# Optimization experiments

Measured on AMD Instinct MI355X. Metric: run time of the kernel, lower is better.

## Reference

```python
import jax, jax.numpy as jnp
import numpy as np

B, C, N, K, R, PART = 2, 64, 16384, 16, 16, 6
_reps = [C // PART] * (PART - 1) + [C - (C // PART) * (PART - 1)]
_RIDX = np.repeat(np.arange(PART), _reps)  # torch.repeat_interleave index map (6 -> C)


def setup_inputs() -> dict:
    key = jax.random.key(0)
    ks = jax.random.split(key, 26)
    f = lambda i, sh: jax.random.normal(ks[i], sh, jnp.float32)
    u = lambda i, sh: jax.random.uniform(ks[i], sh, jnp.float32, 0.5, 1.5)
    return {
        'x': f(0, (B, C, N)),
        'xyz': f(1, (B, 3, N)) * 0.5,
        'idx': jax.random.randint(ks[2], (B, N, K), 0, N),
        'w3a': f(3, (C, 1, 3, 3, 3)) * 0.1, 'b3a': f(4, (C,)) * 0.1,
        'g3a': u(5, (C,)), 'be3a': f(6, (C,)) * 0.1, 'm3a': f(7, (C,)) * 0.1, 'v3a': u(8, (C,)),
        'w3b': f(9, (C, 1, 3, 3, 3)) * 0.1, 'b3b': f(10, (C,)) * 0.1,
        'g3b': u(11, (C,)), 'be3b': f(12, (C,)) * 0.1, 'm3b': f(13, (C,)) * 0.1, 'v3b': u(14, (C,)),
        'wp1': f(15, (3, C)) * 0.1, 'gp': u(16, (3,)), 'bp': f(17, (3,)) * 0.1,
        'mp': f(18, (3,)) * 0.1, 'vp': u(19, (3,)),
        'wp2': f(20, (3, 3)) * 0.3,
        'gt': u(21, (C,)), 'bt': f(22, (C,)) * 0.1, 'mt': f(23, (C,)) * 0.1, 'vt': u(24, (C,)),
    }


def _bn(x, g, b, m, v, eps):
    sh = (1, -1) + (1,) * (x.ndim - 2)
    return (x - m.reshape(sh)) * (g.reshape(sh) * jax.lax.rsqrt(v.reshape(sh) + eps)) + b.reshape(sh)


def _lrelu(x):
    return jnp.where(x > 0, x, 0.1 * x)


def _forward(x, xyz, idx, w3a, b3a, g3a, be3a, m3a, v3a, w3b, b3b, g3b, be3b, m3b, v3b,
             wp1, gp, bp, mp, vp, wp2, gt, bt, mt, vt):
    # --- voxelization: scatter-average points into R^3 grid (PVCNN, normalize=False) ---
    nc = jnp.clip((xyz - xyz.mean(axis=2, keepdims=True) + 1.0) * 0.5 * R, 0.0, R - 1.0)  # [B,3,N]
    vi = jnp.round(nc).astype(jnp.int32)
    flat = (vi[:, 0] * R + vi[:, 1]) * R + vi[:, 2]  # [B,N]
    seg = lambda fe, s: jax.ops.segment_sum(fe, s, num_segments=R ** 3)
    sums = jax.vmap(lambda xb, sb: seg(xb.T, sb))(x, flat)                    # [B,R^3,C]
    cnts = jax.vmap(lambda sb: seg(jnp.ones((N,), x.dtype), sb))(flat)        # [B,R^3]
    grid = (sums / jnp.maximum(cnts, 1.0)[..., None]).transpose(0, 2, 1).reshape(B, C, R, R, R)
    # --- depthwise 3x3x3 conv3d -> BN3d(eps=1e-4) -> LeakyReLU(0.1), twice ---
    dn = ('NCDHW', 'OIDHW', 'NCDHW')
    h = jax.lax.conv_general_dilated(grid, w3a, (1, 1, 1), 'SAME', dimension_numbers=dn,
                                     feature_group_count=C) + b3a.reshape(1, C, 1, 1, 1)
    h = _lrelu(_bn(h, g3a, be3a, m3a, v3a, 1e-4))
    h = jax.lax.conv_general_dilated(h, w3b, (1, 1, 1), 'SAME', dimension_numbers=dn,
                                     feature_group_count=C) + b3b.reshape(1, C, 1, 1, 1)
    h = _lrelu(_bn(h, g3b, be3b, m3b, v3b, 1e-4))
    # --- trilinear devoxelize: gather 8 corners with trilinear weights ---
    gridf = h.reshape(B, C, R * R * R)
    c0 = jnp.floor(nc).astype(jnp.int32)
    c1 = jnp.minimum(c0 + 1, R - 1)
    fr = nc - c0.astype(nc.dtype)
    p_v_x = jnp.zeros((B, C, N), x.dtype)
    for dx in (0, 1):
        for dy in (0, 1):
            for dz in (0, 1):
                ix = c1[:, 0] if dx else c0[:, 0]
                iy = c1[:, 1] if dy else c0[:, 1]
                iz = c1[:, 2] if dz else c0[:, 2]
                w = ((fr[:, 0] if dx else 1 - fr[:, 0]) *
                     (fr[:, 1] if dy else 1 - fr[:, 1]) *
                     (fr[:, 2] if dz else 1 - fr[:, 2]))  # [B,N]
                fi = (ix * R + iy) * R + iz
                p_v_x = p_v_x + jnp.take_along_axis(gridf, fi[:, None, :], axis=2) * w[:, None, :]
    # --- point branch: gather K neighbors by precomputed ball-query idx ---
    x_j = jnp.take_along_axis(x[:, :, None, :], idx[:, None, :, :], axis=3)      # [B,C,N,K]
    xyz_j = jnp.take_along_axis(xyz[:, :, None, :], idx[:, None, :, :], axis=3)  # [B,3,N,K]
    dp1 = xyz_j - xyz[:, :, :, None]                                             # [B,3,N,K]
    df = x_j - x[:, :, :, None]                                                  # [B,C,N,K]
    # proj_conv: 1x1 conv C->3, BN2d(eps=1e-5), ReLU, 1x1 conv 3->3
    t = jax.nn.relu(_bn(jnp.einsum('oc,bcnk->bonk', wp1, df), gp, bp, mp, vp, 1e-5))
    dp2 = jnp.einsum('op,bpnk->bonk', wp2, t)
    dp = jnp.concatenate([dp1, dp2], axis=1)   # [B,6,N,K]
    wgt = dp[:, _RIDX]                         # repeat_interleave(6 -> C)
    x_j = jax.nn.relu(_bn(x_j * wgt, gt, bt, mt, vt, 1e-5))  # proj_transform
    p_p_x = jnp.max(x_j, axis=-1)              # max-pool over neighbors
    return p_v_x + p_p_x                       # agg_way == 'add'


def reference(x, xyz, idx, w3a, b3a, g3a, be3a, m3a, v3a, w3b, b3b, g3b, be3b, m3b, v3b,
              wp1, gp, bp, mp, vp, wp2, gt, bt, mt, vt):
    return _forward(x, xyz, idx, w3a, b3a, g3a, be3a, m3a, v3a, w3b, b3b, g3b, be3b, m3b, v3b,
                    wp1, gp, bp, mp, vp, wp2, gt, bt, mt, vt)
```

## Files before the change

kernel.cpp:

```cpp
#include <hip/hip_runtime.h>
#include <math.h>

#define BB 2
#define CC 64
#define NPTS 16384
#define KK 16
#define RR 16
#define R3 4096

__device__ __forceinline__ unsigned short f2b(float f) {
  unsigned int u = __float_as_uint(f);
  unsigned int r = u + 0x7fffu + ((u >> 16) & 1u);
  return (unsigned short)(r >> 16);
}
__device__ __forceinline__ float b2f(unsigned short h) {
  return __uint_as_float(((unsigned int)h) << 16);
}

__global__ __launch_bounds__(256) void k_mean(const float* __restrict__ xyz,
                                              float* __restrict__ meanv,
                                              float4* __restrict__ zbase,
                                              int zcount4) {
  int gt = blockIdx.x * 256 + threadIdx.x;
  int stride = gridDim.x * 256;
  for (int i = gt; i < zcount4; i += stride)
    zbase[i] = make_float4(0.f, 0.f, 0.f, 0.f);

  if (blockIdx.x < 6) {
    int row = blockIdx.x;
    const float* src = xyz + (size_t)row * NPTS;
    float s = 0.f;
    for (int i = threadIdx.x; i < NPTS; i += 256) s += src[i];
    for (int off = 32; off; off >>= 1) s += __shfl_down(s, off, 64);
    __shared__ float ls[4];
    int lane = threadIdx.x & 63, wv = threadIdx.x >> 6;
    if (lane == 0) ls[wv] = s;
    __syncthreads();
    if (threadIdx.x == 0) meanv[row] = (ls[0] + ls[1] + ls[2] + ls[3]) / (float)NPTS;
  }
}

__global__ void k_voxel(const float* __restrict__ xyz, const float* __restrict__ meanv,
                        float* __restrict__ cnts, int* __restrict__ flat,
                        float* __restrict__ ncT, float* __restrict__ rec) {
  int p = blockIdx.x * 256 + threadIdx.x;
  int b = p / NPTS, n = p % NPTS;
  int vi[3];
#pragma unroll
  for (int o = 0; o < 3; ++o) {
    float v = xyz[((size_t)b * 3 + o) * NPTS + n];
    float t = (v - meanv[b * 3 + o] + 1.0f) * 0.5f * (float)RR;
    t = fminf(fmaxf(t, 0.f), (float)(RR - 1));
    vi[o] = (int)rintf(t);
    rec[(size_t)p * 8 + o] = v;
    ncT[(size_t)p * 4 + o] = t;
  }
  ncT[(size_t)p * 4 + 3] = 0.f;
  int f = (vi[0] * RR + vi[1]) * RR + vi[2];
  flat[p] = f;
  atomicAdd(&cnts[b * R3 + f], 1.0f);
}

__global__ __launch_bounds__(256) void k_transpose(
    const float* __restrict__ x, const int* __restrict__ flat,
    const float* __restrict__ wp1, float* __restrict__ sumsVC,
    unsigned short* __restrict__ xTb, float* __restrict__ rec) {
  __shared__ float tile[64][65];
  __shared__ int lflat[64];
  int bi = blockIdx.x;
  int b = bi >> 8, n0 = (bi & 255) * 64;
  int t = threadIdx.x;
  int nl = t & 63, cq = t >> 6;
  if (t < 64) lflat[t] = flat[b * NPTS + n0 + t];
#pragma unroll 4
  for (int it = 0; it < 16; ++it) {
    int c = it * 4 + cq;
    tile[c][nl] = x[((size_t)b * CC + c) * NPTS + n0 + nl];
  }
  __syncthreads();
  int cw = t & 63, nq = t >> 6;
#pragma unroll 4
  for (int it = 0; it < 16; ++it) {
    int n2 = it * 4 + nq;
    xTb[((size_t)(b * NPTS + n0 + n2)) * 64 + cw] = f2b(tile[cw][n2]);
  }
  int wv = t >> 6, lane = t & 63;
#pragma unroll 2
  for (int i = 0; i < 16; ++i) {
    int n2 = wv * 16 + i;
    atomicAdd(&sumsVC[((size_t)b * R3 + lflat[n2]) * 64 + lane], tile[lane][n2]);
  }
  if (t < 192) {
    int pt = t & 63, o = t >> 6;
    const float* wr = wp1 + o * 64;
    float s = 0.f;
#pragma unroll 8
    for (int c = 0; c < 64; ++c) s += wr[c] * tile[c][pt];
    rec[((size_t)(b * NPTS + n0 + pt)) * 8 + 3 + o] = s;
  }
}

__global__ __launch_bounds__(256) void k_conv(
    const float* __restrict__ sumsVC, const float* __restrict__ cnts,
    const float* __restrict__ w3a, const float* __restrict__ b3a,
    const float* __restrict__ g3a, const float* __restrict__ be3a,
    const float* __restrict__ m3a, const float* __restrict__ v3a,
    const float* __restrict__ w3b, const float* __restrict__ b3b,
    const float* __restrict__ g3b, const float* __restrict__ be3b,
    const float* __restrict__ m3b, const float* __restrict__ v3b,
    unsigned short* __restrict__ gridb) {
  __shared__ float A[5832];
  __shared__ float Bf[5832];
  int bi = blockIdx.x, b = bi >> 6, c = bi & 63;
  int t = threadIdx.x;
  for (int i = t; i < 5832; i += 256) { A[i] = 0.f; Bf[i] = 0.f; }
  __syncthreads();
  const float* cp = cnts + (size_t)b * R3;
  for (int v = t; v < R3; v += 256) {
    int d = v >> 8, h = (v >> 4) & 15, w = v & 15;
    float s = sumsVC[((size_t)b * R3 + v) * 64 + c];
    A[((d + 1) * 18 + (h + 1)) * 18 + (w + 1)] = s / fmaxf(cp[v], 1.0f);
  }
  float wa[27];
#pragma unroll
  for (int i = 0; i < 27; ++i) wa[i] = w3a[c * 27 + i];
  float biasa = b3a[c];
  float sa = g3a[c] * rsqrtf(v3a[c] + 1e-4f);
  float ma = m3a[c], bna = be3a[c];
  __syncthreads();
  for (int v = t; v < R3; v += 256) {
    int d = v >> 8, h = (v >> 4) & 15, w = v & 15;
    int base = (d * 18 + h) * 18 + w;
    float s = 0.f;
#pragma unroll
    for (int kd = 0; kd < 3; ++kd)
#pragma unroll
      for (int kh = 0; kh < 3; ++kh)
#pragma unroll
        for (int kw = 0; kw < 3; ++kw)
          s += wa[kd * 9 + kh * 3 + kw] * A[base + kd * 324 + kh * 18 + kw];
    s += biasa;
    s = (s - ma) * sa + bna;
    s = s > 0.f ? s : 0.1f * s;
    Bf[((d + 1) * 18 + (h + 1)) * 18 + (w + 1)] = s;
  }
  float wb[27];
#pragma unroll
  for (int i = 0; i < 27; ++i) wb[i] = w3b[c * 27 + i];
  float biasb = b3b[c];
  float sb = g3b[c] * rsqrtf(v3b[c] + 1e-4f);
  float mb = m3b[c], bnb = be3b[c];
  __syncthreads();
  for (int v = t; v < R3; v += 256) {
    int d = v >> 8, h = (v >> 4) & 15, w = v & 15;
    int base = (d * 18 + h) * 18 + w;
    float s = 0.f;
#pragma unroll
    for (int kd = 0; kd < 3; ++kd)
#pragma unroll
      for (int kh = 0; kh < 3; ++kh)
#pragma unroll
        for (int kw = 0; kw < 3; ++kw)
          s += wb[kd * 9 + kh * 3 + kw] * Bf[base + kd * 324 + kh * 18 + kw];
    s += biasb;
    s = (s - mb) * sb + bnb;
    s = s > 0.f ? s : 0.1f * s;
    gridb[((size_t)b * R3 + v) * 64 + c] = f2b(s);
  }
}

__global__ __launch_bounds__(256) void k_final(
    const unsigned short* __restrict__ xTb, const float* __restrict__ rec,
    const float* __restrict__ ncT, const unsigned short* __restrict__ gridb,
    const int* __restrict__ idx,
    const float* __restrict__ gp, const float* __restrict__ bp,
    const float* __restrict__ mp, const float* __restrict__ vp,
    const float* __restrict__ wp2,
    const float* __restrict__ gt, const float* __restrict__ bt,
    const float* __restrict__ mt, const float* __restrict__ vt,
    float* __restrict__ out) {
  __shared__ float wgt[16 * 16 * 7];
  __shared__ float res[64][17];
  int t = threadIdx.x;
  int c = t & 63, wv = t >> 6;
  int bid = blockIdx.x;
  int xcd = bid & 7;
  int b = xcd >> 2;
  int grp = (bid >> 3) * 4 + (xcd & 3);
  int p0 = b * NPTS + grp * 16;
  int bBase = b * NPTS;
  const float4* rec4 = (const float4*)rec;

  {
    int pl = t >> 4, k = t & 15;
    int p = p0 + pl;
    int j = idx[(size_t)p * 16 + k];
    float4 r0 = rec4[(size_t)p * 2], r1 = rec4[(size_t)p * 2 + 1];
    int pj = bBase + j;
    float4 q0 = rec4[(size_t)pj * 2], q1 = rec4[(size_t)pj * 2 + 1];
    float sp0 = gp[0] * rsqrtf(vp[0] + 1e-5f);
    float sp1 = gp[1] * rsqrtf(vp[1] + 1e-5f);
    float sp2 = gp[2] * rsqrtf(vp[2] + 1e-5f);
    float d0 = q0.x - r0.x, d1 = q0.y - r0.y, d2 = q0.z - r0.z;
    float e0 = q0.w - r0.w, e1 = q1.x - r1.x, e2 = q1.y - r1.y;
    float t0 = fmaxf((e0 - mp[0]) * sp0 + bp[0], 0.f);
    float t1 = fmaxf((e1 - mp[1]) * sp1 + bp[1], 0.f);
    float t2 = fmaxf((e2 - mp[2]) * sp2 + bp[2], 0.f);
    float* wp = &wgt[(pl * 16 + k) * 7];
    wp[0] = d0; wp[1] = d1; wp[2] = d2;
    wp[3] = wp2[0] * t0 + wp2[1] * t1 + wp2[2] * t2;
    wp[4] = wp2[3] * t0 + wp2[4] * t1 + wp2[5] * t2;
    wp[5] = wp2[6] * t0 + wp2[7] * t1 + wp2[8] * t2;
    ((int*)wp)[6] = j;
  }

  float st = gt[c] * rsqrtf(vt[c] + 1e-5f);
  float mtc = mt[c], btc = bt[c];
  int part = c / 10; if (part > 5) part = 5;
  const float4* nc4 = (const float4*)ncT;
  const unsigned short* gbase = gridb + (size_t)b * R3 * 64;
  __syncthreads();

#pragma unroll
  for (int pi = 0; pi < 4; ++pi) {
    int pl = wv * 4 + pi;
    int p = p0 + pl;
    float4 ncv = nc4[p];
    float c0x = floorf(ncv.x), c0y = floorf(ncv.y), c0z = floorf(ncv.z);
    int i0x = (int)c0x, i0y = (int)c0y, i0z = (int)c0z;
    int i1x = min(i0x + 1, 15), i1y = min(i0y + 1, 15), i1z = min(i0z + 1, 15);
    float fx = ncv.x - c0x, fy = ncv.y - c0y, fz = ncv.z - c0z;
    float pv = 0.f;
#pragma unroll
    for (int dx = 0; dx < 2; ++dx)
#pragma unroll
      for (int dy = 0; dy < 2; ++dy)
#pragma unroll
        for (int dz = 0; dz < 2; ++dz) {
          int ix = dx ? i1x : i0x, iy = dy ? i1y : i0y, iz = dz ? i1z : i0z;
          float wg = (dx ? fx : 1.f - fx) * (dy ? fy : 1.f - fy) * (dz ? fz : 1.f - fz);
          pv += wg * b2f(gbase[(size_t)((ix * 16 + iy) * 16 + iz) * 64 + c]);
        }
    const float* wrow = &wgt[pl * 16 * 7];
    int jv[16];
#pragma unroll
    for (int k = 0; k < 16; ++k) jv[k] = ((const int*)wrow)[k * 7 + 6];
    unsigned short xv[16];
#pragma unroll
    for (int k = 0; k < 16; ++k) xv[k] = xTb[((size_t)(bBase + jv[k])) * 64 + c];
    float acc = -1e30f;
#pragma unroll
    for (int k = 0; k < 16; ++k) {
      float w = wrow[k * 7 + part];
      float v = fmaxf((b2f(xv[k]) * w - mtc) * st + btc, 0.f);
      acc = fmaxf(acc, v);
    }
    res[c][pl] = pv + acc;
  }
  __syncthreads();
  int n0 = grp * 16;
  int i = t & 15, crow = t >> 4;
#pragma unroll
  for (int r2 = 0; r2 < 4; ++r2) {
    int ccw = crow + r2 * 16;
    out[((size_t)b * CC + ccw) * NPTS + n0 + i] = res[ccw][i];
  }
}

extern "C" void kernel_launch(void* const* d_in, const int* in_sizes, int n_in,
                              void* d_out, int out_size, void* d_ws, size_t ws_size,
                              hipStream_t stream) {
  const float* x    = (const float*)d_in[0];
  const float* xyz  = (const float*)d_in[1];
  const int*   idx  = (const int*)d_in[2];
  const float* w3a  = (const float*)d_in[3];
  const float* b3a  = (const float*)d_in[4];
  const float* g3a  = (const float*)d_in[5];
  const float* be3a = (const float*)d_in[6];
  const float* m3a  = (const float*)d_in[7];
  const float* v3a  = (const float*)d_in[8];
  const float* w3b  = (const float*)d_in[9];
  const float* b3b  = (const float*)d_in[10];
  const float* g3b  = (const float*)d_in[11];
  const float* be3b = (const float*)d_in[12];
  const float* m3b  = (const float*)d_in[13];
  const float* v3b  = (const float*)d_in[14];
  const float* wp1  = (const float*)d_in[15];
  const float* gp   = (const float*)d_in[16];
  const float* bp   = (const float*)d_in[17];
  const float* mp   = (const float*)d_in[18];
  const float* vp   = (const float*)d_in[19];
  const float* wp2  = (const float*)d_in[20];
  const float* gt   = (const float*)d_in[21];
  const float* bt   = (const float*)d_in[22];
  const float* mt   = (const float*)d_in[23];
  const float* vt   = (const float*)d_in[24];

  float* ws     = (float*)d_ws;
  float* sumsVC = ws;
  float* cnts   = sumsVC + 524288;
  float* meanv  = cnts + 8192;
  int*   flat   = (int*)(meanv + 8);
  float* ncT    = (float*)(flat + 32768);
  float* rec    = ncT + 131072;
  unsigned short* xTb   = (unsigned short*)(rec + 262144);
  unsigned short* gridb = xTb + 2097152;

  k_mean<<<128, 256, 0, stream>>>(xyz, meanv, (float4*)sumsVC, 133120);
  k_voxel<<<(BB * NPTS) / 256, 256, 0, stream>>>(xyz, meanv, cnts, flat, ncT, rec);
  k_transpose<<<(BB * NPTS) / 64, 256, 0, stream>>>(x, flat, wp1, sumsVC, xTb, rec);
  k_conv<<<BB * CC, 256, 0, stream>>>(sumsVC, cnts, w3a, b3a, g3a, be3a, m3a, v3a,
                                      w3b, b3b, g3b, be3b, m3b, v3b, gridb);
  k_final<<<(BB * NPTS) / 16, 256, 0, stream>>>(xTb, rec, ncT, gridb, idx,
                                                gp, bp, mp, vp, wp2,
                                                gt, bt, mt, vt, (float*)d_out);
}
```

Before: 74.62 us.

## Fuse voxelization into transpose, split conv by depth halves, widen final tiles

Folds the per-point voxelization (count atomics, normalized coords, rec xyz) into the transpose kernel, which removes one launch and the flat index buffer. Splits the depthwise conv into two depth halves per channel using compact halo slabs, doubling the block count and shrinking shared memory. The final kernel now handles 32 points per block instead of 16, halving the grid. Together these aim to cut launch overhead and raise occupancy and parallelism in the conv stage, at the cost of recomputing halo slices in the conv.

```diff
diff --git a/kernel.cpp b/kernel.cpp
--- a/kernel.cpp
+++ b/kernel.cpp
@@ -17,10 +17,10 @@
   return __uint_as_float(((unsigned int)h) << 16);
 }
 
-__global__ __launch_bounds__(256) void k_mean(const float* __restrict__ xyz,
-                                              float* __restrict__ meanv,
-                                              float4* __restrict__ zbase,
-                                              int zcount4) {
+__global__ __launch_bounds__(256) void k_zero_mean(const float* __restrict__ xyz,
+                                                   float* __restrict__ meanv,
+                                                   float4* __restrict__ zbase,
+                                                   int zcount4) {
   int gt = blockIdx.x * 256 + threadIdx.x;
   int stride = gridDim.x * 256;
   for (int i = gt; i < zcount4; i += stride)
@@ -40,38 +40,38 @@
   }
 }
 
-__global__ void k_voxel(const float* __restrict__ xyz, const float* __restrict__ meanv,
-                        float* __restrict__ cnts, int* __restrict__ flat,
-                        float* __restrict__ ncT, float* __restrict__ rec) {
-  int p = blockIdx.x * 256 + threadIdx.x;
-  int b = p / NPTS, n = p % NPTS;
-  int vi[3];
-#pragma unroll
-  for (int o = 0; o < 3; ++o) {
-    float v = xyz[((size_t)b * 3 + o) * NPTS + n];
-    float t = (v - meanv[b * 3 + o] + 1.0f) * 0.5f * (float)RR;
-    t = fminf(fmaxf(t, 0.f), (float)(RR - 1));
-    vi[o] = (int)rintf(t);
-    rec[(size_t)p * 8 + o] = v;
-    ncT[(size_t)p * 4 + o] = t;
-  }
-  ncT[(size_t)p * 4 + 3] = 0.f;
-  int f = (vi[0] * RR + vi[1]) * RR + vi[2];
-  flat[p] = f;
-  atomicAdd(&cnts[b * R3 + f], 1.0f);
-}
-
-__global__ __launch_bounds__(256) void k_transpose(
-    const float* __restrict__ x, const int* __restrict__ flat,
-    const float* __restrict__ wp1, float* __restrict__ sumsVC,
-    unsigned short* __restrict__ xTb, float* __restrict__ rec) {
+__global__ __launch_bounds__(256) void k_prep(
+    const float* __restrict__ x, const float* __restrict__ xyz,
+    const float* __restrict__ meanv, const float* __restrict__ wp1,
+    float* __restrict__ sumsVC, float* __restrict__ cnts,
+    unsigned short* __restrict__ xTb, float* __restrict__ rec,
+    float* __restrict__ ncT) {
   __shared__ float tile[64][65];
   __shared__ int lflat[64];
   int bi = blockIdx.x;
   int b = bi >> 8, n0 = (bi & 255) * 64;
   int t = threadIdx.x;
+
+  if (t < 64) {
+    int n = n0 + t;
+    int p = b * NPTS + n;
+    float vv[3]; int vi[3];
+#pragma unroll
+    for (int o = 0; o < 3; ++o) {
+      float v = xyz[((size_t)b * 3 + o) * NPTS + n];
+      float tc = (v - meanv[b * 3 + o] + 1.0f) * 0.5f * (float)RR;
+      tc = fminf(fmaxf(tc, 0.f), (float)(RR - 1));
+      vv[o] = tc;
+      vi[o] = (int)rintf(tc);
+      rec[(size_t)p * 8 + o] = v;
+    }
+    int f = (vi[0] * RR + vi[1]) * RR + vi[2];
+    lflat[t] = f;
+    atomicAdd(&cnts[b * R3 + f], 1.0f);
+    ((float4*)ncT)[p] = make_float4(vv[0], vv[1], vv[2], 0.f);
+  }
+
   int nl = t & 63, cq = t >> 6;
-  if (t < 64) lflat[t] = flat[b * NPTS + n0 + t];
 #pragma unroll 4
   for (int it = 0; it < 16; ++it) {
     int c = it * 4 + cq;
@@ -109,63 +109,95 @@
     const float* __restrict__ g3b, const float* __restrict__ be3b,
     const float* __restrict__ m3b, const float* __restrict__ v3b,
     unsigned short* __restrict__ gridb) {
-  __shared__ float A[5832];
-  __shared__ float Bf[5832];
-  int bi = blockIdx.x, b = bi >> 6, c = bi & 63;
+  __shared__ float A[12 * 256];
+  __shared__ float Ba[10 * 256];
+  int bi = blockIdx.x;
+  int b = bi >> 7, rem = bi & 127, c = rem >> 1, half = rem & 1;
+  int d0 = half * 8;
   int t = threadIdx.x;
-  for (int i = t; i < 5832; i += 256) { A[i] = 0.f; Bf[i] = 0.f; }
-  __syncthreads();
+
   const float* cp = cnts + (size_t)b * R3;
-  for (int v = t; v < R3; v += 256) {
-    int d = v >> 8, h = (v >> 4) & 15, w = v & 15;
-    float s = sumsVC[((size_t)b * R3 + v) * 64 + c];
-    A[((d + 1) * 18 + (h + 1)) * 18 + (w + 1)] = s / fmaxf(cp[v], 1.0f);
-  }
-  float wa[27];
-#pragma unroll
-  for (int i = 0; i < 27; ++i) wa[i] = w3a[c * 27 + i];
-  float biasa = b3a[c];
-  float sa = g3a[c] * rsqrtf(v3a[c] + 1e-4f);
-  float ma = m3a[c], bna = be3a[c];
-  __syncthreads();
-  for (int v = t; v < R3; v += 256) {
-    int d = v >> 8, h = (v >> 4) & 15, w = v & 15;
-    int base = (d * 18 + h) * 18 + w;
-    float s = 0.f;
-#pragma unroll
-    for (int kd = 0; kd < 3; ++kd)
-#pragma unroll
-      for (int kh = 0; kh < 3; ++kh)
-#pragma unroll
-        for (int kw = 0; kw < 3; ++kw)
-          s += wa[kd * 9 + kh * 3 + kw] * A[base + kd * 324 + kh * 18 + kw];
-    s += biasa;
-    s = (s - ma) * sa + bna;
-    s = s > 0.f ? s : 0.1f * s;
-    Bf[((d + 1) * 18 + (h + 1)) * 18 + (w + 1)] = s;
-  }
-  float wb[27];
-#pragma unroll
-  for (int i = 0; i < 27; ++i) wb[i] = w3b[c * 27 + i];
-  float biasb = b3b[c];
-  float sb = g3b[c] * rsqrtf(v3b[c] + 1e-4f);
-  float mb = m3b[c], bnb = be3b[c];
-  __syncthreads();
-  for (int v = t; v < R3; v += 256) {
-    int d = v >> 8, h = (v >> 4) & 15, w = v & 15;
-    int base = (d * 18 + h) * 18 + w;
-    float s = 0.f;
-#pragma unroll
-    for (int kd = 0; kd < 3; ++kd)
-#pragma unroll
-      for (int kh = 0; kh < 3; ++kh)
-#pragma unroll
-        for (int kw = 0; kw < 3; ++kw)
-          s += wb[kd * 9 + kh * 3 + kw] * Bf[base + kd * 324 + kh * 18 + kw];
-    s += biasb;
-    s = (s - mb) * sb + bnb;
-    s = s > 0.f ? s : 0.1f * s;
-    gridb[((size_t)b * R3 + v) * 64 + c] = f2b(s);
+#pragma unroll
+  for (int it = 0; it < 12; ++it) {
+    int i = t + it * 256;
+    int s = it, hw = t;
+    int da = d0 - 2 + s;
+    float val = 0.f;
+    if ((unsigned)da < 16u) {
+      int v = (da << 8) + hw;
+      val = sumsVC[((size_t)b * R3 + v) * 64 + c] / fmaxf(cp[v], 1.0f);
+    }
+    A[i] = val;
+  }
+  float wk[27];
+#pragma unroll
+  for (int i = 0; i < 27; ++i) wk[i] = w3a[c * 27 + i];
+  float bias = b3a[c];
+  float sc = g3a[c] * rsqrtf(v3a[c] + 1e-4f);
+  float mn = m3a[c], bt2 = be3a[c];
+  __syncthreads();
+#pragma unroll
+  for (int it = 0; it < 10; ++it) {
+    int s = it;
+    int da = d0 - 1 + s;
+    int h = t >> 4, w = t & 15;
+    float out = 0.f;
+    if ((unsigned)da < 16u) {
+      float acc = 0.f;
+#pragma unroll
+      for (int kd = 0; kd < 3; ++kd) {
+        const float* Asl = &A[(s + kd) * 256];
+#pragma unroll
+        for (int kh = 0; kh < 3; ++kh) {
+          int hh = h + kh - 1;
+          if ((unsigned)hh < 16u) {
+#pragma unroll
+            for (int kw = 0; kw < 3; ++kw) {
+              int ww = w + kw - 1;
+              if ((unsigned)ww < 16u)
+                acc += wk[kd * 9 + kh * 3 + kw] * Asl[(hh << 4) + ww];
+            }
+          }
+        }
+      }
+      acc += bias;
+      acc = (acc - mn) * sc + bt2;
+      out = acc > 0.f ? acc : 0.1f * acc;
+    }
+    Ba[s * 256 + t] = out;
+  }
+#pragma unroll
+  for (int i = 0; i < 27; ++i) wk[i] = w3b[c * 27 + i];
+  bias = b3b[c];
+  sc = g3b[c] * rsqrtf(v3b[c] + 1e-4f);
+  mn = m3b[c]; bt2 = be3b[c];
+  __syncthreads();
+#pragma unroll
+  for (int it = 0; it < 8; ++it) {
+    int s = it;
+    int db = d0 + s;
+    int h = t >> 4, w = t & 15;
+    float acc = 0.f;
+#pragma unroll
+    for (int kd = 0; kd < 3; ++kd) {
+      const float* Bsl = &Ba[(s + kd) * 256];
+#pragma unroll
+      for (int kh = 0; kh < 3; ++kh) {
+        int hh = h + kh - 1;
+        if ((unsigned)hh < 16u) {
+#pragma unroll
+          for (int kw = 0; kw < 3; ++kw) {
+            int ww = w + kw - 1;
+            if ((unsigned)ww < 16u)
+              acc += wk[kd * 9 + kh * 3 + kw] * Bsl[(hh << 4) + ww];
+          }
+        }
+      }
+    }
+    acc += bias;
+    acc = (acc - mn) * sc + bt2;
+    acc = acc > 0.f ? acc : 0.1f * acc;
+    gridb[((size_t)b * R3 + (db << 8) + t) * 64 + c] = f2b(acc);
   }
 }
 
@@ -179,51 +211,57 @@
     const float* __restrict__ gt, const float* __restrict__ bt,
     const float* __restrict__ mt, const float* __restrict__ vt,
     float* __restrict__ out) {
-  __shared__ float wgt[16 * 16 * 7];
-  __shared__ float res[64][17];
+  __shared__ float wgt[32 * 16 * 7];
+  __shared__ float res[64][33];
   int t = threadIdx.x;
-  int c = t & 63, wv = t >> 6;
-  int bid = blockIdx.x;
-  int xcd = bid & 7;
-  int b = xcd >> 2;
-  int grp = (bid >> 3) * 4 + (xcd & 3);
-  int p0 = b * NPTS + grp * 16;
+  int g = blockIdx.x;
+  int b = (g & 7) >> 2;
+  int w = ((g >> 3) << 2) + (g & 3);
+  int n0 = w * 32;
+  int p0 = b * NPTS + n0;
   int bBase = b * NPTS;
   const float4* rec4 = (const float4*)rec;
 
   {
-    int pl = t >> 4, k = t & 15;
-    int p = p0 + pl;
-    int j = idx[(size_t)p * 16 + k];
-    float4 r0 = rec4[(size_t)p * 2], r1 = rec4[(size_t)p * 2 + 1];
-    int pj = bBase + j;
-    float4 q0 = rec4[(size_t)pj * 2], q1 = rec4[(size_t)pj * 2 + 1];
     float sp0 = gp[0] * rsqrtf(vp[0] + 1e-5f);
     float sp1 = gp[1] * rsqrtf(vp[1] + 1e-5f);
     float sp2 = gp[2] * rsqrtf(vp[2] + 1e-5f);
-    float d0 = q0.x - r0.x, d1 = q0.y - r0.y, d2 = q0.z - r0.z;
-    float e0 = q0.w - r0.w, e1 = q1.x - r1.x, e2 = q1.y - r1.y;
-    float t0 = fmaxf((e0 - mp[0]) * sp0 + bp[0], 0.f);
-    float t1 = fmaxf((e1 - mp[1]) * sp1 + bp[1], 0.f);
-    float t2 = fmaxf((e2 - mp[2]) * sp2 + bp[2], 0.f);
-    float* wp = &wgt[(pl * 16 + k) * 7];
-    wp[0] = d0; wp[1] = d1; wp[2] = d2;
-    wp[3] = wp2[0] * t0 + wp2[1] * t1 + wp2[2] * t2;
-    wp[4] = wp2[3] * t0 + wp2[4] * t1 + wp2[5] * t2;
-    wp[5] = wp2[6] * t0 + wp2[7] * t1 + wp2[8] * t2;
-    ((int*)wp)[6] = j;
-  }
-
+    float mp0 = mp[0], mp1 = mp[1], mp2 = mp[2];
+    float bp0 = bp[0], bp1 = bp[1], bp2 = bp[2];
+#pragma unroll
+    for (int it = 0; it < 2; ++it) {
+      int pair = t + it * 256;
+      int pl = pair >> 4, k = pair & 15;
+      int p = p0 + pl;
+      int j = idx[(size_t)p * 16 + k];
+      float4 r0 = rec4[(size_t)p * 2], r1 = rec4[(size_t)p * 2 + 1];
+      int pj = bBase + j;
+      float4 q0 = rec4[(size_t)pj * 2], q1 = rec4[(size_t)pj * 2 + 1];
+      float d0 = q0.x - r0.x, d1 = q0.y - r0.y, d2 = q0.z - r0.z;
+      float e0 = q0.w - r0.w, e1 = q1.x - r1.x, e2 = q1.y - r1.y;
+      float t0 = fmaxf((e0 - mp0) * sp0 + bp0, 0.f);
+      float t1 = fmaxf((e1 - mp1) * sp1 + bp1, 0.f);
+      float t2 = fmaxf((e2 - mp2) * sp2 + bp2, 0.f);
+      float* wp = &wgt[pair * 7];
+      wp[0] = d0; wp[1] = d1; wp[2] = d2;
+      wp[3] = wp2[0] * t0 + wp2[1] * t1 + wp2[2] * t2;
+      wp[4] = wp2[3] * t0 + wp2[4] * t1 + wp2[5] * t2;
+      wp[5] = wp2[6] * t0 + wp2[7] * t1 + wp2[8] * t2;
+      ((int*)wp)[6] = j;
+    }
+  }
+  __syncthreads();
+
+  int c = t & 63, wv = t >> 6;
   float st = gt[c] * rsqrtf(vt[c] + 1e-5f);
   float mtc = mt[c], btc = bt[c];
   int part = c / 10; if (part > 5) part = 5;
   const float4* nc4 = (const float4*)ncT;
   const unsigned short* gbase = gridb + (size_t)b * R3 * 64;
-  __syncthreads();
-
-#pragma unroll
-  for (int pi = 0; pi < 4; ++pi) {
-    int pl = wv * 4 + pi;
+
+#pragma unroll
+  for (int pi = 0; pi < 8; ++pi) {
+    int pl = wv * 8 + pi;
     int p = p0 + pl;
     float4 ncv = nc4[p];
     float c0x = floorf(ncv.x), c0y = floorf(ncv.y), c0z = floorf(ncv.z);
@@ -248,22 +286,21 @@
     unsigned short xv[16];
 #pragma unroll
     for (int k = 0; k < 16; ++k) xv[k] = xTb[((size_t)(bBase + jv[k])) * 64 + c];
-    float acc = -1e30f;
+    float a = -1e30f;
 #pragma unroll
     for (int k = 0; k < 16; ++k) {
-      float w = wrow[k * 7 + part];
-      float v = fmaxf((b2f(xv[k]) * w - mtc) * st + btc, 0.f);
-      acc = fmaxf(acc, v);
-    }
-    res[c][pl] = pv + acc;
-  }
-  __syncthreads();
-  int n0 = grp * 16;
-  int i = t & 15, crow = t >> 4;
-#pragma unroll
-  for (int r2 = 0; r2 < 4; ++r2) {
-    int ccw = crow + r2 * 16;
-    out[((size_t)b * CC + ccw) * NPTS + n0 + i] = res[ccw][i];
+      float w2 = wrow[k * 7 + part];
+      float v = fmaxf((b2f(xv[k]) * w2 - mtc) * st + btc, 0.f);
+      a = fmaxf(a, v);
+    }
+    res[c][pl] = pv + a;
+  }
+  __syncthreads();
+  int col = t & 31, rq = t >> 5;
+#pragma unroll
+  for (int r = 0; r < 8; ++r) {
+    int row = rq + r * 8;
+    out[((size_t)(b * CC + row)) * NPTS + n0 + col] = res[row][col];
   }
 }
 
@@ -300,18 +337,16 @@
   float* sumsVC = ws;
   float* cnts   = sumsVC + 524288;
   float* meanv  = cnts + 8192;
-  int*   flat   = (int*)(meanv + 8);
-  float* ncT    = (float*)(flat + 32768);
+  float* ncT    = meanv + 8;
   float* rec    = ncT + 131072;
   unsigned short* xTb   = (unsigned short*)(rec + 262144);
   unsigned short* gridb = xTb + 2097152;
 
-  k_mean<<<128, 256, 0, stream>>>(xyz, meanv, (float4*)sumsVC, 133120);
-  k_voxel<<<(BB * NPTS) / 256, 256, 0, stream>>>(xyz, meanv, cnts, flat, ncT, rec);
-  k_transpose<<<(BB * NPTS) / 64, 256, 0, stream>>>(x, flat, wp1, sumsVC, xTb, rec);
-  k_conv<<<BB * CC, 256, 0, stream>>>(sumsVC, cnts, w3a, b3a, g3a, be3a, m3a, v3a,
-                                      w3b, b3b, g3b, be3b, m3b, v3b, gridb);
-  k_final<<<(BB * NPTS) / 16, 256, 0, stream>>>(xTb, rec, ncT, gridb, idx,
-                                                gp, bp, mp, vp, wp2,
-                                                gt, bt, mt, vt, (float*)d_out);
-}
+  k_zero_mean<<<128, 256, 0, stream>>>(xyz, meanv, (float4*)sumsVC, 133120);
+  k_prep<<<512, 256, 0, stream>>>(x, xyz, meanv, wp1, sumsVC, cnts, xTb, rec, ncT);
+  k_conv<<<256, 256, 0, stream>>>(sumsVC, cnts, w3a, b3a, g3a, be3a, m3a, v3a,
+                                  w3b, b3b, g3b, be3b, m3b, v3b, gridb);
+  k_final<<<1024, 256, 0, stream>>>(xTb, rec, ncT, gridb, idx,
+                                    gp, bp, mp, vp, wp2,
+                                    gt, bt, mt, vt, (float*)d_out);
+}
```

After: 79.59 us. 1.07x slower.
